# Kernel optimization log

Hardware: AMD Instinct MI355X
Metric: run time of the kernel (lower is better)

The kernel has to match this reference:

```python
import jax, jax.numpy as jnp
import numpy as np

B, S, D, E, R, TOP_K = 4, 4096, 1024, 10, 4, 2
SCALING = 1.0 / R  # alpha / rank


def setup_inputs() -> dict:
    key = jax.random.key(0)
    ks = jax.random.split(key, 7)
    return {
        "x": jax.random.normal(ks[0], (B, S, D), dtype=jnp.float32),
        "W_base": jax.random.normal(ks[1], (D, D), dtype=jnp.float32) * (D ** -0.5),
        "b_base": jax.random.normal(ks[2], (D,), dtype=jnp.float32) * 0.02,
        "gate_W": jax.random.normal(ks[3], (E, D), dtype=jnp.float32) * (D ** -0.5),
        "gate_b": jax.random.normal(ks[4], (E,), dtype=jnp.float32) * 0.02,
        "lora_down": jax.random.normal(ks[5], (E, R, D), dtype=jnp.float32) * (D ** -0.5),
        "lora_up": jax.random.normal(ks[6], (E, D, R), dtype=jnp.float32) * (R ** -0.5),
    }


def reference(x, W_base, b_base, gate_W, gate_b, lora_down, lora_up):
    # Base (frozen) linear: [B,S,D]
    base_out = jnp.einsum("bsd,od->bso", x, W_base) + b_base

    # Top-k gating: logits [B,S,E] -> sparse softmax weights [B,S,E]
    logits = jnp.einsum("bsd,ed->bse", x, gate_W) + gate_b
    top_vals, top_idx = jax.lax.top_k(logits, TOP_K)          # [B,S,K]
    top_w = jax.nn.softmax(top_vals, axis=-1)                 # [B,S,K]
    # scatter top-k weights back to dense [B,S,E] (non-top-k are zero)
    weights = jnp.sum(top_w[..., None] * jax.nn.one_hot(top_idx, E, dtype=x.dtype), axis=-2)

    # All-expert LoRA (matches original loop); weight in rank space to avoid
    # materializing [B,S,E,D]: sum_e w_e * up_e(down_e(x)) * scaling
    h = jnp.einsum("bsd,erd->bser", x, lora_down)             # [B,S,E,R]
    h = h * weights[..., None]
    lora_out = jnp.einsum("bser,edr->bsd", h, lora_up) * SCALING

    return base_out + lora_out
```

## Files before the change

### kernel.cpp

```cpp
#include <hip/hip_runtime.h>
#include <hip/hip_bf16.h>
#include <cstdint>
#include <cstddef>

#define D_DIM 1024
#define E_NUM 10

typedef __attribute__((ext_vector_type(8))) short bf16x8;
typedef __attribute__((ext_vector_type(4))) float f32x4;
typedef unsigned short u16;
typedef unsigned int u32;

__device__ __forceinline__ u16 f2bf(float f) {
  union { float f; u32 u; } v; v.f = f;
  u32 r = v.u + 0x7fffu + ((v.u >> 16) & 1u);
  return (u16)(r >> 16);
}
__device__ __forceinline__ float bf2f(u16 u) {
  union { u32 u; float f; } v; v.u = ((u32)u) << 16; return v.f;
}
__device__ __forceinline__ float dot4(float4 a, float4 b) {
  return a.x * b.x + a.y * b.y + a.z * b.z + a.w * b.w;
}

__global__ void conv_w(const float* __restrict__ W, u16* __restrict__ Wb) {
  const int i = (blockIdx.x * 256 + threadIdx.x) * 8;
  float4 a = *(const float4*)(W + i);
  float4 b = *(const float4*)(W + i + 4);
  *(ushort4*)(Wb + i)     = make_ushort4(f2bf(a.x), f2bf(a.y), f2bf(a.z), f2bf(a.w));
  *(ushort4*)(Wb + i + 4) = make_ushort4(f2bf(b.x), f2bf(b.y), f2bf(b.z), f2bf(b.w));
}

__global__ void prep_ldb(const float* __restrict__ ld, u16* __restrict__ Bld) {
  const int r = blockIdx.x;
  for (int c = threadIdx.x; c < D_DIM; c += 256)
    Bld[r * D_DIM + c] = (r < 40) ? f2bf(ld[r * D_DIM + c]) : (u16)0;
}

__global__ void prep_ub(const float* __restrict__ lup, u16* __restrict__ Ub) {
  const int g = blockIdx.x * 256 + threadIdx.x;
  const int o = g >> 6, j = g & 63;
  Ub[g] = (j < 40) ? f2bf(lup[(size_t)(j >> 2) * (D_DIM * 4) + o * 4 + (j & 3)]) : (u16)0;
}

__global__ __launch_bounds__(256)
void moe_prep_h(const float* __restrict__ x, const u16* __restrict__ Bld,
                u16* __restrict__ hb, u16* __restrict__ xb) {
  __shared__ u16 sX[4][16 * 64];
  __shared__ u16 sB[4][48 * 64];
  __shared__ float sP[4][3][16][17];

  const int tid = threadIdx.x, lane = tid & 63, w = tid >> 6;
  const int r0 = blockIdx.x * 16;
  const int kbase = w * 256;

  f32x4 acc[3] = {};

  float4 av[4];
#pragma unroll
  for (int i = 0; i < 2; ++i) {
    const int c = lane * 2 + i, row = c >> 3, kc = c & 7;
    const float* g = x + (size_t)(r0 + row) * D_DIM + kbase + kc * 8;
    av[i * 2]     = *(const float4*)g;
    av[i * 2 + 1] = *(const float4*)(g + 4);
  }

#pragma unroll 1
  for (int kt = 0; kt < 4; ++kt) {
    const int k0 = kbase + kt * 64;
#pragma unroll
    for (int i = 0; i < 6; ++i) {
      const int c = i * 64 + lane, row = c >> 3, kc = (c & 7) ^ (row & 7);
      __builtin_amdgcn_global_load_lds(
          (const __attribute__((address_space(1))) u32*)(Bld + (size_t)row * D_DIM + k0 + kc * 8),
          (__attribute__((address_space(3))) u32*)&sB[w][c * 8], 16, 0, 0);
    }
#pragma unroll
    for (int i = 0; i < 2; ++i) {
      const int c = lane * 2 + i, row = c >> 3, kc = c & 7;
      const float4 a = av[i * 2], b = av[i * 2 + 1];
      const ushort4 ha  = make_ushort4(f2bf(a.x), f2bf(a.y), f2bf(a.z), f2bf(a.w));
      const ushort4 hb4 = make_ushort4(f2bf(b.x), f2bf(b.y), f2bf(b.z), f2bf(b.w));
      const int off = (row * 128 + kc * 16) ^ ((row & 7) << 4);
      *(ushort4*)((char*)sX[w] + off)     = ha;
      *(ushort4*)((char*)sX[w] + off + 8) = hb4;
      if (xb) {
        u16* dst = xb + (size_t)(r0 + row) * D_DIM + k0 + kc * 8;
        *(ushort4*)dst       = ha;
        *(ushort4*)(dst + 4) = hb4;
      }
    }
    __syncthreads();
    if (kt < 3) {
#pragma unroll
      for (int i = 0; i < 2; ++i) {
        const int c = lane * 2 + i, row = c >> 3, kc = c & 7;
        const float* g = x + (size_t)(r0 + row) * D_DIM + (k0 + 64) + kc * 8;
        av[i * 2]     = *(const float4*)g;
        av[i * 2 + 1] = *(const float4*)(g + 4);
      }
    }
#pragma unroll
    for (int kk = 0; kk < 2; ++kk) {
      const int kb = kk * 64 + ((lane >> 4) * 16);
      const int rA = lane & 15;
      const bf16x8 a0 = *(const bf16x8*)((const char*)sX[w] + ((rA * 128 + kb) ^ ((rA & 7) << 4)));
#pragma unroll
      for (int cf = 0; cf < 3; ++cf) {
        const int rB = cf * 16 + (lane & 15);
        const bf16x8 q = *(const bf16x8*)((const char*)sB[w] + ((rB * 128 + kb) ^ ((rB & 7) << 4)));
        acc[cf] = __builtin_amdgcn_mfma_f32_16x16x32_bf16(a0, q, acc[cf], 0, 0, 0);
      }
    }
    __syncthreads();
  }

#pragma unroll
  for (int cf = 0; cf < 3; ++cf)
#pragma unroll
    for (int j = 0; j < 4; ++j)
      sP[w][cf][(lane >> 4) * 4 + j][lane & 15] = acc[cf][j];
  __syncthreads();

  const int row = tid >> 4, c16 = tid & 15;
#pragma unroll
  for (int cf = 0; cf < 3; ++cf) {
    const int col = cf * 16 + c16;
    if (col < 40) {
      const float s = sP[0][cf][row][c16] + sP[1][cf][row][c16] +
                      sP[2][cf][row][c16] + sP[3][cf][row][c16];
      hb[(size_t)(r0 + row) * 40 + col] = f2bf(s);
    }
  }
}

__global__ __launch_bounds__(256)
void moe_gate3(const float* __restrict__ x, const float* __restrict__ gW,
               const float* __restrict__ gb, const u16* __restrict__ hb,
               u16* __restrict__ cd) {
  __shared__ char  sRaw[4][4096];
  __shared__ float sPart[16 * 16 * 11];

  const int tid = threadIdx.x, lane = tid & 63, w = tid >> 6;
  const int r0 = blockIdx.x * 16;
  const int kq = w * 256;
  const int t = lane & 15, s = lane >> 4;

  float acc[E_NUM] = {};

  float4 pv[4];
#pragma unroll
  for (int i = 0; i < 4; ++i) {
    const int f = i * 64 + lane, tok = f >> 4, g = f & 15;
    pv[i] = *(const float4*)(x + (size_t)(r0 + tok) * D_DIM + kq + g * 4);
  }

#pragma unroll 1
  for (int c = 0; c < 4; ++c) {
    const int k0 = kq + c * 64;
#pragma unroll
    for (int i = 0; i < 4; ++i) {
      const int f = i * 64 + lane, tok = f >> 4, g = f & 15;
      *(float4*)(sRaw[w] + tok * 256 + ((g ^ (tok & 15)) << 4)) = pv[i];
    }
    float4 xr[4];
#pragma unroll
    for (int j = 0; j < 4; ++j) {
      const int g = s * 4 + j;
      xr[j] = *(const float4*)(sRaw[w] + t * 256 + ((g ^ (t & 15)) << 4));
    }
    if (c < 3) {
#pragma unroll
      for (int i = 0; i < 4; ++i) {
        const int f = i * 64 + lane, tok = f >> 4, g = f & 15;
        pv[i] = *(const float4*)(x + (size_t)(r0 + tok) * D_DIM + (k0 + 64) + g * 4);
      }
    }
    const float* gwk = gW + k0 + s * 16;
#pragma unroll
    for (int e = 0; e < E_NUM; ++e) {
      float v = acc[e];
#pragma unroll
      for (int j = 0; j < 4; ++j)
        v += dot4(xr[j], *(const float4*)(gwk + e * D_DIM + j * 4));
      acc[e] = v;
    }
  }

  {
    float* dst = sPart + ((w * 4 + s) * 16 + t) * 11;
#pragma unroll
    for (int e = 0; e < E_NUM; ++e) dst[e] = acc[e];
  }
  __syncthreads();

  if (tid < 16) {
    const int tok = tid, tt = r0 + tok;
    float lg[E_NUM];
#pragma unroll
    for (int e = 0; e < E_NUM; ++e) {
      float v = gb[e];
#pragma unroll
      for (int p = 0; p < 16; ++p) v += sPart[(p * 16 + tok) * 11 + e];
      lg[e] = v;
    }
    int e0 = 0; float v0 = lg[0];
#pragma unroll
    for (int e = 1; e < E_NUM; ++e) if (lg[e] > v0) { v0 = lg[e]; e0 = e; }
    int e1 = -1; float v1 = -3.0e38f;
#pragma unroll
    for (int e = 0; e < E_NUM; ++e) if (e != e0 && lg[e] > v1) { v1 = lg[e]; e1 = e; }
    const float pp = expf(v1 - v0);
    const float inv = 1.f / (1.f + pp);
    const float s0 = inv * 0.25f, s1 = pp * inv * 0.25f;

    u16* dst = cd + (size_t)tt * 64;
    const u16* hrow = hb + (size_t)tt * 40;
#pragma unroll
    for (int e = 0; e < E_NUM; ++e) {
      const float we = (e == e0) ? s0 : ((e == e1) ? s1 : 0.f);
      const ushort4 hh = *(const ushort4*)(hrow + e * 4);
      *(ushort4*)(dst + e * 4) = make_ushort4(
          f2bf(bf2f(hh.x) * we), f2bf(bf2f(hh.y) * we),
          f2bf(bf2f(hh.z) * we), f2bf(bf2f(hh.w) * we));
    }
#pragma unroll
    for (int j = 40; j < 64; j += 4)
      *(ushort4*)(dst + j) = make_ushort4(0, 0, 0, 0);
  }
}

__global__ __launch_bounds__(256, 2)
void moe_gemm_t(const u16* __restrict__ xb, const u16* __restrict__ Wbf,
                const u16* __restrict__ cd, const u16* __restrict__ Ub,
                const float* __restrict__ bias, float* __restrict__ out) {
  __shared__ u16 Al[2][128 * 64];
  __shared__ u16 Bl[2][128 * 64];

  const int tid = threadIdx.x, lane = tid & 63, wid = tid >> 6;
  const int wm = wid >> 1, wn = wid & 1;
  const int p = blockIdx.x;
  const int cx = p & 7, q = p >> 3;
  const int nb = q & 7, mb = cx * 16 + (q >> 3);
  const int m0 = mb * 128, n0 = nb * 128;

  int sc_row[4], sc_kc[4];
#pragma unroll
  for (int i = 0; i < 4; ++i) {
    const int c = i * 256 + tid;
    sc_row[i] = c >> 3;
    sc_kc[i]  = (c & 7) ^ (sc_row[i] & 7);
  }

  f32x4 acc[4][4] = {};

  auto STAGE = [&](int buf, int ktile) {
    const u16* As; const u16* Bs; size_t str; int ko;
    if (ktile < 16) {
      As = xb + (size_t)m0 * D_DIM; Bs = Wbf + (size_t)n0 * D_DIM;
      str = D_DIM; ko = ktile * 64;
    } else {
      As = cd + (size_t)m0 * 64; Bs = Ub + (size_t)n0 * 64;
      str = 64; ko = 0;
    }
#pragma unroll
    for (int i = 0; i < 4; ++i) {
      const int c = i * 256 + tid;
      __builtin_amdgcn_global_load_lds(
          (const __attribute__((address_space(1))) u32*)(As + (size_t)sc_row[i] * str + ko + sc_kc[i] * 8),
          (__attribute__((address_space(3))) u32*)&Al[buf][c * 8], 16, 0, 0);
    }
#pragma unroll
    for (int i = 0; i < 4; ++i) {
      const int c = i * 256 + tid;
      __builtin_amdgcn_global_load_lds(
          (const __attribute__((address_space(1))) u32*)(Bs + (size_t)sc_row[i] * str + ko + sc_kc[i] * 8),
          (__attribute__((address_space(3))) u32*)&Bl[buf][c * 8], 16, 0, 0);
    }
  };

  STAGE(0, 0);
  __syncthreads();

#pragma unroll 1
  for (int kt = 0; kt < 17; ++kt) {
    const int cur = kt & 1;
    if (kt < 16) STAGE(cur ^ 1, kt + 1);
#pragma unroll
    for (int kk = 0; kk < 2; ++kk) {
      bf16x8 af[4], bfr[4];
      const int kb = kk * 64 + ((lane >> 4) * 16);
#pragma unroll
      for (int m = 0; m < 4; ++m) {
        const int row = wm * 64 + m * 16 + (lane & 15);
        af[m] = *(const bf16x8*)((const char*)Al[cur] + ((row * 128 + kb) ^ ((row & 7) << 4)));
      }
#pragma unroll
      for (int n = 0; n < 4; ++n) {
        const int row = wn * 64 + n * 16 + (lane & 15);
        bfr[n] = *(const bf16x8*)((const char*)Bl[cur] + ((row * 128 + kb) ^ ((row & 7) << 4)));
      }
#pragma unroll
      for (int m = 0; m < 4; ++m)
#pragma unroll
        for (int n = 0; n < 4; ++n)
          acc[m][n] = __builtin_amdgcn_mfma_f32_16x16x32_bf16(af[m], bfr[n], acc[m][n], 0, 0, 0);
    }
    __syncthreads();
  }

  const int rg = lane >> 4, cl = lane & 15;
  const int baser = m0 + wm * 64, basec = n0 + wn * 64;
  float bs[4];
#pragma unroll
  for (int n = 0; n < 4; ++n) bs[n] = bias[basec + n * 16 + cl];
#pragma unroll
  for (int m = 0; m < 4; ++m)
#pragma unroll
    for (int j = 0; j < 4; ++j) {
      const int rr = baser + m * 16 + rg * 4 + j;
#pragma unroll
      for (int n = 0; n < 4; ++n)
        out[(size_t)rr * D_DIM + basec + n * 16 + cl] = acc[m][n][j] + bs[n];
    }
}

extern "C" void kernel_launch(void* const* d_in, const int* in_sizes, int n_in,
                              void* d_out, int out_size, void* d_ws, size_t ws_size,
                              hipStream_t stream) {
  const float* x   = (const float*)d_in[0];
  const float* Wb_ = (const float*)d_in[1];
  const float* bb  = (const float*)d_in[2];
  const float* gW  = (const float*)d_in[3];
  const float* gb  = (const float*)d_in[4];
  const float* ld  = (const float*)d_in[5];
  const float* lup = (const float*)d_in[6];

  char* w = (char*)d_ws;
  u16* Wbf = (u16*)w;
  u16* Ub  = (u16*)(w + 2048ull * 1024);
  u16* Bld = (u16*)(w + 2176ull * 1024);
  u16* cd  = (u16*)(w + 2272ull * 1024);
  u16* hb  = (u16*)(w + 4320ull * 1024);
  u16* xb  = (u16*)(w + 5600ull * 1024);

  hipLaunchKernelGGL(conv_w,     dim3(512),  dim3(256), 0, stream, Wb_, Wbf);
  hipLaunchKernelGGL(prep_ldb,   dim3(48),   dim3(256), 0, stream, ld, Bld);
  hipLaunchKernelGGL(prep_ub,    dim3(256),  dim3(256), 0, stream, lup, Ub);
  hipLaunchKernelGGL(moe_prep_h, dim3(1024), dim3(256), 0, stream, x, Bld, hb, xb);
  hipLaunchKernelGGL(moe_gate3,  dim3(1024), dim3(256), 0, stream, x, gW, gb, hb, cd);
  hipLaunchKernelGGL(moe_gemm_t, dim3(1024), dim3(256), 0, stream,
                     xb, Wbf, cd, Ub, bb, (float*)d_out);
}
```

Baseline: 119.7 us.

## Enlarge GEMM tile to 256x256 with 8 waves and split-phase pipelined prefetch

Replaces the 128x128, 4-wave GEMM with a 256x256 tile using 8 waves of 512 threads. Each wave computes 128x64, and the MFMA work is split into two halves, with the next-next k-tile staged into the freed buffer between them, using explicit vmcnt waits, raw barriers and setprio. The larger tile cuts global/L2 traffic per FLOP and overlaps loads with compute. In exchange, LDS use doubles to 128KB per block, there are only 256 blocks, accumulator register pressure rises, and occupancy may drop.

```diff
diff --git a/kernel.cpp b/kernel.cpp
--- a/kernel.cpp
+++ b/kernel.cpp
@@ -230,92 +230,122 @@
   }
 }
 
-__global__ __launch_bounds__(256, 2)
-void moe_gemm_t(const u16* __restrict__ xb, const u16* __restrict__ Wbf,
-                const u16* __restrict__ cd, const u16* __restrict__ Ub,
-                const float* __restrict__ bias, float* __restrict__ out) {
-  __shared__ u16 Al[2][128 * 64];
-  __shared__ u16 Bl[2][128 * 64];
+__global__ __launch_bounds__(512, 2)
+void moe_gemm_8p(const u16* __restrict__ xb, const u16* __restrict__ Wbf,
+                 const u16* __restrict__ cd, const u16* __restrict__ Ub,
+                 const float* __restrict__ bias, float* __restrict__ out) {
+  __shared__ u16 Al[2][256 * 64];
+  __shared__ u16 Bl[2][256 * 64];
 
   const int tid = threadIdx.x, lane = tid & 63, wid = tid >> 6;
-  const int wm = wid >> 1, wn = wid & 1;
+  const int wm = wid >> 2, wn = wid & 3;
   const int p = blockIdx.x;
   const int cx = p & 7, q = p >> 3;
-  const int nb = q & 7, mb = cx * 16 + (q >> 3);
-  const int m0 = mb * 128, n0 = nb * 128;
-
-  int sc_row[4], sc_kc[4];
-#pragma unroll
-  for (int i = 0; i < 4; ++i) {
-    const int c = i * 256 + tid;
-    sc_row[i] = c >> 3;
-    sc_kc[i]  = (c & 7) ^ (sc_row[i] & 7);
-  }
-
-  f32x4 acc[4][4] = {};
+  const int nb = q & 3, mb = cx * 8 + (q >> 2);
+  const int m0 = mb * 256, n0 = nb * 256;
+
+  const int hA = tid >> 8;
+  const int ltA = tid & 255;
+  const int hB = (wid >> 1) & 1;
+  const int ltB = ((wid >> 2) * 2 + (wid & 1)) * 64 + lane;
+
+  f32x4 acc[8][4] = {};
 
   auto STAGE = [&](int buf, int ktile) {
-    const u16* As; const u16* Bs; size_t str; int ko;
-    if (ktile < 16) {
-      As = xb + (size_t)m0 * D_DIM; Bs = Wbf + (size_t)n0 * D_DIM;
-      str = D_DIM; ko = ktile * 64;
-    } else {
-      As = cd + (size_t)m0 * 64; Bs = Ub + (size_t)n0 * 64;
-      str = 64; ko = 0;
-    }
 #pragma unroll
     for (int i = 0; i < 4; ++i) {
-      const int c = i * 256 + tid;
+      const int c = i * 256 + ltA, row = c >> 3, kc = (c & 7) ^ (row & 7);
+      const u16* src = (ktile < 16)
+          ? xb + (size_t)(m0 + hA * 128 + row) * D_DIM + ktile * 64 + kc * 8
+          : cd + (size_t)(m0 + hA * 128 + row) * 64 + kc * 8;
       __builtin_amdgcn_global_load_lds(
-          (const __attribute__((address_space(1))) u32*)(As + (size_t)sc_row[i] * str + ko + sc_kc[i] * 8),
-          (__attribute__((address_space(3))) u32*)&Al[buf][c * 8], 16, 0, 0);
+          (const __attribute__((address_space(1))) u32*)src,
+          (__attribute__((address_space(3))) u32*)&Al[buf][hA * 8192 + c * 8], 16, 0, 0);
     }
 #pragma unroll
     for (int i = 0; i < 4; ++i) {
-      const int c = i * 256 + tid;
+      const int c = i * 256 + ltB, row = c >> 3, kc = (c & 7) ^ (row & 7);
+      const u16* src = (ktile < 16)
+          ? Wbf + (size_t)(n0 + hB * 128 + row) * D_DIM + ktile * 64 + kc * 8
+          : Ub + (size_t)(n0 + hB * 128 + row) * 64 + kc * 8;
       __builtin_amdgcn_global_load_lds(
-          (const __attribute__((address_space(1))) u32*)(Bs + (size_t)sc_row[i] * str + ko + sc_kc[i] * 8),
-          (__attribute__((address_space(3))) u32*)&Bl[buf][c * 8], 16, 0, 0);
+          (const __attribute__((address_space(1))) u32*)src,
+          (__attribute__((address_space(3))) u32*)&Bl[buf][hB * 8192 + c * 8], 16, 0, 0);
     }
   };
 
   STAGE(0, 0);
-  __syncthreads();
+  STAGE(1, 1);
+  asm volatile("s_waitcnt vmcnt(8)" ::: "memory");
+  __builtin_amdgcn_s_barrier();
 
 #pragma unroll 1
   for (int kt = 0; kt < 17; ++kt) {
     const int cur = kt & 1;
-    if (kt < 16) STAGE(cur ^ 1, kt + 1);
-#pragma unroll
-    for (int kk = 0; kk < 2; ++kk) {
-      bf16x8 af[4], bfr[4];
-      const int kb = kk * 64 + ((lane >> 4) * 16);
-#pragma unroll
-      for (int m = 0; m < 4; ++m) {
-        const int row = wm * 64 + m * 16 + (lane & 15);
-        af[m] = *(const bf16x8*)((const char*)Al[cur] + ((row * 128 + kb) ^ ((row & 7) << 4)));
-      }
-#pragma unroll
-      for (int n = 0; n < 4; ++n) {
-        const int row = wn * 64 + n * 16 + (lane & 15);
-        bfr[n] = *(const bf16x8*)((const char*)Bl[cur] + ((row * 128 + kb) ^ ((row & 7) << 4)));
-      }
+    const int kbq = (lane >> 4) * 16;
+
+    bf16x8 bfr[4][2], af0[4][2];
+#pragma unroll
+    for (int n = 0; n < 4; ++n) {
+      const int row = wn * 64 + n * 16 + (lane & 15);
+#pragma unroll
+      for (int kk = 0; kk < 2; ++kk)
+        bfr[n][kk] = *(const bf16x8*)((const char*)Bl[cur] +
+                        ((row * 128 + kk * 64 + kbq) ^ ((row & 7) << 4)));
+    }
+#pragma unroll
+    for (int m = 0; m < 4; ++m) {
+      const int row = wm * 128 + m * 16 + (lane & 15);
+#pragma unroll
+      for (int kk = 0; kk < 2; ++kk)
+        af0[m][kk] = *(const bf16x8*)((const char*)Al[cur] +
+                        ((row * 128 + kk * 64 + kbq) ^ ((row & 7) << 4)));
+    }
+#pragma unroll
+    for (int kk = 0; kk < 2; ++kk)
 #pragma unroll
       for (int m = 0; m < 4; ++m)
 #pragma unroll
         for (int n = 0; n < 4; ++n)
-          acc[m][n] = __builtin_amdgcn_mfma_f32_16x16x32_bf16(af[m], bfr[n], acc[m][n], 0, 0, 0);
-    }
-    __syncthreads();
+          acc[m][n] = __builtin_amdgcn_mfma_f32_16x16x32_bf16(af0[m][kk], bfr[n][kk], acc[m][n], 0, 0, 0);
+
+    bf16x8 af1[4][2];
+#pragma unroll
+    for (int m = 0; m < 4; ++m) {
+      const int row = wm * 128 + (m + 4) * 16 + (lane & 15);
+#pragma unroll
+      for (int kk = 0; kk < 2; ++kk)
+        af1[m][kk] = *(const bf16x8*)((const char*)Al[cur] +
+                        ((row * 128 + kk * 64 + kbq) ^ ((row & 7) << 4)));
+    }
+    asm volatile("s_waitcnt lgkmcnt(0)" ::: "memory");
+    __builtin_amdgcn_sched_barrier(0);
+    __builtin_amdgcn_s_barrier();
+    if (kt + 2 <= 16) STAGE(cur, kt + 2);
+
+    __builtin_amdgcn_s_setprio(1);
+#pragma unroll
+    for (int kk = 0; kk < 2; ++kk)
+#pragma unroll
+      for (int m = 0; m < 4; ++m)
+#pragma unroll
+        for (int n = 0; n < 4; ++n)
+          acc[m + 4][n] = __builtin_amdgcn_mfma_f32_16x16x32_bf16(af1[m][kk], bfr[n][kk], acc[m + 4][n], 0, 0, 0);
+    __builtin_amdgcn_s_setprio(0);
+
+    if (kt < 15)      { asm volatile("s_waitcnt vmcnt(8)" ::: "memory"); }
+    else if (kt < 16) { asm volatile("s_waitcnt vmcnt(0)" ::: "memory"); }
+    __builtin_amdgcn_sched_barrier(0);
+    __builtin_amdgcn_s_barrier();
   }
 
   const int rg = lane >> 4, cl = lane & 15;
-  const int baser = m0 + wm * 64, basec = n0 + wn * 64;
+  const int baser = m0 + wm * 128, basec = n0 + wn * 64;
   float bs[4];
 #pragma unroll
   for (int n = 0; n < 4; ++n) bs[n] = bias[basec + n * 16 + cl];
 #pragma unroll
-  for (int m = 0; m < 4; ++m)
+  for (int m = 0; m < 8; ++m)
 #pragma unroll
     for (int j = 0; j < 4; ++j) {
       const int rr = baser + m * 16 + rg * 4 + j;
@@ -349,6 +379,6 @@
   hipLaunchKernelGGL(prep_ub,    dim3(256),  dim3(256), 0, stream, lup, Ub);
   hipLaunchKernelGGL(moe_prep_h, dim3(1024), dim3(256), 0, stream, x, Bld, hb, xb);
   hipLaunchKernelGGL(moe_gate3,  dim3(1024), dim3(256), 0, stream, x, gW, gb, hb, cd);
-  hipLaunchKernelGGL(moe_gemm_t, dim3(1024), dim3(256), 0, stream,
+  hipLaunchKernelGGL(moe_gemm_8p, dim3(256), dim3(512), 0, stream,
                      xb, Wbf, cd, Ub, bb, (float*)d_out);
 }
```

Measured after the change: 151.0 us. 26.1% more time.
